# Optimization experiments

Hardware: AMD Instinct MI355X
Metric: run time of the kernel (lower is better)

Reference implementation:

```python
import jax, jax.numpy as jnp
import numpy as np

B, T, N, F = 32, 64, 128, 128
U, K1, K2 = 64, 64, 32
EPS = 1e-3  # keras BatchNormalization default epsilon
SLOPE = 0.01  # LeakyReLU negative_slope


def setup_inputs() -> dict:
    key = jax.random.key(0)
    ks = jax.random.split(key, 16)
    g = lambda k, sh, s=0.05: jax.random.normal(k, sh, dtype=jnp.float32) * s
    inp = {
        "x": jax.random.normal(ks[0], (B, T, F), dtype=jnp.float32),
        "a": jax.random.uniform(ks[1], (B, N, N), dtype=jnp.float32),
        # LSTM (keras gate order i, f, c, o)
        "lstm_k": g(ks[2], (F, 4 * U)),
        "lstm_r": g(ks[3], (U, 4 * U)),
        "lstm_b": jnp.zeros((4 * U,), jnp.float32),
        # BatchNorm params (inference form: gamma, beta, moving mean, moving var)
        "bnl_g": jnp.ones((U,), jnp.float32), "bnl_b": jnp.zeros((U,), jnp.float32),
        "bnl_m": jnp.zeros((U,), jnp.float32), "bnl_v": jnp.ones((U,), jnp.float32),
        "w1": g(ks[4], (U, K1)), "b1": jnp.zeros((K1,), jnp.float32),
        "bn1_g": jnp.ones((K1,), jnp.float32), "bn1_b": jnp.zeros((K1,), jnp.float32),
        "bn1_m": jnp.zeros((K1,), jnp.float32), "bn1_v": jnp.ones((K1,), jnp.float32),
        "w2": g(ks[5], (K1, K2)), "b2": jnp.zeros((K2,), jnp.float32),
        "bn2_g": jnp.ones((K2,), jnp.float32), "bn2_b": jnp.zeros((K2,), jnp.float32),
        "bn2_m": jnp.zeros((K2,), jnp.float32), "bn2_v": jnp.ones((K2,), jnp.float32),
        "d1_w": g(ks[6], (T * N * K2, 3), 0.01), "d1_b": jnp.zeros((3,), jnp.float32),
        "d2_w": g(ks[7], (3, N)), "d2_b": jnp.zeros((N,), jnp.float32),
    }
    return inp


def _bn(x, g, b, m, v):
    return (x - m) * (g * jax.lax.rsqrt(v + EPS)) + b


def _leaky(x):
    return jnp.where(x >= 0, x, SLOPE * x)


def _lstm(x, Wk, Wr, b):
    # x: [B, T, F] -> hs: [B, T, U]
    xz = jnp.einsum('btf,fg->btg', x, Wk) + b  # precompute input projections
    u = Wr.shape[0]
    h0 = jnp.zeros((x.shape[0], u), x.dtype)
    c0 = jnp.zeros((x.shape[0], u), x.dtype)

    def step(carry, zt):
        h, c = carry
        z = zt + h @ Wr
        i, f, g_, o = jnp.split(z, 4, axis=-1)
        i = jax.nn.sigmoid(i); f = jax.nn.sigmoid(f)
        g_ = jnp.tanh(g_); o = jax.nn.sigmoid(o)
        c = f * c + i * g_
        h = o * jnp.tanh(c)
        return (h, c), h

    _, hs = jax.lax.scan(step, (h0, c0), xz.transpose(1, 0, 2))
    return hs.transpose(1, 0, 2)


def reference(x, a, lstm_k, lstm_r, lstm_b, bnl_g, bnl_b, bnl_m, bnl_v,
              w1, b1, bn1_g, bn1_b, bn1_m, bn1_v,
              w2, b2, bn2_g, bn2_b, bn2_m, bn2_v,
              d1_w, d1_b, d2_w, d2_b):
    h = _lstm(x, lstm_k, lstm_r, lstm_b)              # [B, T, U]
    h = _bn(h, bnl_g, bnl_b, bnl_m, bnl_v)            # inference BN; dropout is identity
    # tile each timestep's LSTM output over the N nodes, then GCN1
    support1 = jnp.einsum('btu,uk->btk', h, w1)       # [B, T, K1] (identical across nodes)
    sup1 = jnp.broadcast_to(support1[:, :, None, :], (h.shape[0], h.shape[1], N, w1.shape[1]))
    g1 = jnp.einsum('bij,btjk->btik', a, sup1) + b1   # adjacency matmul
    g1 = _leaky(g1)
    g1 = _bn(g1, bn1_g, bn1_b, bn1_m, bn1_v)
    # GCN2
    sup2 = jnp.einsum('btnk,km->btnm', g1, w2)
    g2 = jnp.einsum('bij,btjm->btim', a, sup2) + b2
    g2 = _leaky(g2)
    g2 = _bn(g2, bn2_g, bn2_b, bn2_m, bn2_v)          # [B, T, N, K2]
    flat = g2.reshape(g2.shape[0], -1)                # [B, T*N*K2]
    d1 = jax.nn.relu(flat @ d1_w + d1_b)              # [B, 3]
    return d1 @ d2_w + d2_b                           # [B, N]
```

## Files before the change

kernel.cpp:

```cpp
#include <hip/hip_runtime.h>

#define BB 32
#define TT 64
#define NN 128
#define FF 128
#define UU 64
#define K1 64
#define K2 32
#define G4 256
#define EPSV 1e-3f
#define SLOPE 0.01f

#define ALD 136
#define SLD 136
#define WLD 72

typedef __attribute__((ext_vector_type(8))) short short8;
typedef __attribute__((ext_vector_type(4))) float f32x4;
typedef __attribute__((ext_vector_type(2))) __fp16 half2v;

__device__ __forceinline__ float sigmoidf_(float x) {
  return __builtin_amdgcn_rcpf(1.f + __expf(-x));
}
__device__ __forceinline__ float tanhf_(float x) {
  return 1.f - 2.f * __builtin_amdgcn_rcpf(__expf(2.f * x) + 1.f);
}
__device__ __forceinline__ float leaky_(float x) { return x >= 0.f ? x : SLOPE * x; }
__device__ __forceinline__ unsigned short f2bf(float x) {
  union { float f; unsigned u; } v; v.f = x;
  unsigned r = v.u + 0x7fff + ((v.u >> 16) & 1);
  return (unsigned short)(r >> 16);
}

__global__ __launch_bounds__(256) void k_pre(const float* __restrict__ x,
                                             const float* __restrict__ wk,
                                             const float* __restrict__ bias,
                                             const float* __restrict__ a,
                                             const float* __restrict__ w2,
                                             const float* __restrict__ wr,
                                             float* __restrict__ xz,
                                             float* __restrict__ rsum,
                                             unsigned short* __restrict__ apad,
                                             unsigned short* __restrict__ w2t,
                                             unsigned* __restrict__ wrp) {
  int tid = threadIdx.x;
  if (blockIdx.x < 32) {
    int b = blockIdx.x;
    int wave = tid >> 6, lane = tid & 63;
    const float* ab = a + (size_t)b * NN * NN;
    for (int r = 0; r < 32; ++r) {
      int row = wave * 32 + r;
      float2 v = *(const float2*)(ab + (size_t)row * NN + lane * 2);
      float s = v.x + v.y;
#pragma unroll
      for (int off = 32; off >= 1; off >>= 1) s += __shfl_down(s, off);
      if (lane == 0) rsum[b * NN + row] = s;
    }
    unsigned short* ap = apad + (size_t)b * NN * ALD;
    for (int idx = tid; idx < NN * NN; idx += 256) {
      int i = idx >> 7, j = idx & 127;
      ap[i * ALD + j] = f2bf(ab[idx]);
    }
    if (b == 0) {
      for (int idx = tid; idx < K1 * K2; idx += 256) {
        int k = idx >> 5, m = idx & 31;
        w2t[m * WLD + k] = f2bf(w2[idx]);
      }
    }
    if (b == 1) {
      for (int idx = tid; idx < 4 * 32 * UU; idx += 256) {
        int u2 = idx & 63;
        int p = (idx >> 6) & 31;
        int gate = idx >> 11;
        int col = gate * UU + u2;
        union { __fp16 h[2]; unsigned u; } pk;
        pk.h[0] = (__fp16)wr[(2 * p) * G4 + col];
        pk.h[1] = (__fp16)wr[(2 * p + 1) * G4 + col];
        wrp[idx] = pk.u;
      }
    }
  } else {
    __shared__ float xs[8][FF];
    int row0 = (blockIdx.x - 32) * 8;
    for (int i = tid; i < 8 * FF; i += 256) xs[i >> 7][i & 127] = x[(size_t)row0 * FF + i];
    __syncthreads();
    int g = tid;
    float acc[8];
    float bg = bias[g];
#pragma unroll
    for (int r = 0; r < 8; ++r) acc[r] = bg;
    for (int f = 0; f < FF; ++f) {
      float w = wk[f * G4 + g];
#pragma unroll
      for (int r = 0; r < 8; ++r) acc[r] += xs[r][f] * w;
    }
#pragma unroll
    for (int r = 0; r < 8; ++r) xz[(size_t)(row0 + r) * G4 + g] = acc[r];
  }
}

__global__ __launch_bounds__(64, 1) void k_lstm(const float* __restrict__ xz,
                                                const unsigned* __restrict__ wrp,
                                                const float* __restrict__ bnl_g,
                                                const float* __restrict__ bnl_b,
                                                const float* __restrict__ bnl_m,
                                                const float* __restrict__ bnl_v,
                                                float* __restrict__ hbn) {
  __shared__ __align__(16) float xz_lds[TT * G4];
  __shared__ __align__(16) __fp16 h16[UU];
  int u = threadIdx.x;
  int b = blockIdx.x;

  {
    const float4* src = (const float4*)(xz + (size_t)b * TT * G4);
    float4* dst = (float4*)xz_lds;
#pragma unroll
    for (int k = 0; k < 64; ++k) dst[u + k * 64] = src[u + k * 64];
  }
  unsigned wv[4][32];
#pragma unroll
  for (int gate = 0; gate < 4; ++gate)
#pragma unroll
    for (int p = 0; p < 32; ++p) wv[gate][p] = wrp[(gate * 32 + p) * UU + u];

  float bscale = bnl_g[u] * rsqrtf(bnl_v[u] + EPSV);
  float boff = bnl_b[u] - bnl_m[u] * bscale;
  h16[u] = (__fp16)0.f;
  float c = 0.f;
  float* hb = hbn + (size_t)b * TT * UU;

  for (int t = 0; t < TT; ++t) {
    unsigned hw[32];
    {
      const uint4* hq = (const uint4*)h16;
#pragma unroll
      for (int k = 0; k < 8; ++k) {
        uint4 v = hq[k];
        hw[4 * k + 0] = v.x; hw[4 * k + 1] = v.y; hw[4 * k + 2] = v.z; hw[4 * k + 3] = v.w;
      }
    }
    float zi = xz_lds[t * G4 + u];
    float zf = xz_lds[t * G4 + 64 + u];
    float zg = xz_lds[t * G4 + 128 + u];
    float zo = xz_lds[t * G4 + 192 + u];
#pragma unroll
    for (int p = 0; p < 32; ++p) {
      half2v hh = __builtin_bit_cast(half2v, hw[p]);
      zi = __builtin_amdgcn_fdot2(__builtin_bit_cast(half2v, wv[0][p]), hh, zi, false);
      zf = __builtin_amdgcn_fdot2(__builtin_bit_cast(half2v, wv[1][p]), hh, zf, false);
      zg = __builtin_amdgcn_fdot2(__builtin_bit_cast(half2v, wv[2][p]), hh, zg, false);
      zo = __builtin_amdgcn_fdot2(__builtin_bit_cast(half2v, wv[3][p]), hh, zo, false);
    }
    float i_ = sigmoidf_(zi), f_ = sigmoidf_(zf), g_ = tanhf_(zg), o_ = sigmoidf_(zo);
    c = f_ * c + i_ * g_;
    float h = o_ * tanhf_(c);
    h16[u] = (__fp16)h;
    hb[t * UU + u] = h * bscale + boff;
  }
}

__global__ __launch_bounds__(256) void k_gcn(
    const float* __restrict__ hbn, const float* __restrict__ w1,
    const float* __restrict__ rsum,
    const unsigned short* __restrict__ apad, const unsigned short* __restrict__ w2t,
    const float* __restrict__ b1,
    const float* __restrict__ bn1_g, const float* __restrict__ bn1_b,
    const float* __restrict__ bn1_m, const float* __restrict__ bn1_v,
    const float* __restrict__ b2,
    const float* __restrict__ bn2_g, const float* __restrict__ bn2_b,
    const float* __restrict__ bn2_m, const float* __restrict__ bn2_v,
    const float* __restrict__ d1w, float* __restrict__ part) {
  __shared__ unsigned short a_lds[NN * ALD];
  __shared__ unsigned short s2_lds[K2 * SLD];
  __shared__ unsigned short w2_lds[K2 * WLD];
  __shared__ float4 gp[K1];
  __shared__ float r_lds[NN];
  __shared__ float p2[3 * K2];
  __shared__ float red[12];

  int blk = blockIdx.x;
  int b = blk & 31, t = blk >> 5;
  int tid = threadIdx.x;
  int lane = tid & 63, wave = tid >> 6;
  int l15 = lane & 15, l4 = lane >> 4;

  {
    const uint4* src = (const uint4*)(apad + (size_t)b * NN * ALD);
    uint4* dst = (uint4*)a_lds;
    for (int i = tid; i < NN * ALD / 8; i += 256) dst[i] = src[i];
  }
  {
    const uint2* src = (const uint2*)w2t;
    uint2* dst = (uint2*)w2_lds;
    for (int i = tid; i < K2 * WLD / 4; i += 256) dst[i] = src[i];
  }
  if (tid < K1) {
    float hv = hbn[((size_t)b * TT + t) * UU + tid];
    float s1v = 0.f;
#pragma unroll
    for (int u = 0; u < UU; ++u) s1v += __shfl(hv, u) * w1[u * K1 + tid];
    float s = bn1_g[tid] * rsqrtf(bn1_v[tid] + EPSV);
    gp[tid] = make_float4(s1v, b1[tid], s, bn1_b[tid] - bn1_m[tid] * s);
  }
  if (tid >= 64 && tid < 64 + NN) r_lds[tid - 64] = rsum[b * NN + (tid - 64)];
  if (tid >= 192 && tid < 192 + K2) {
    int m = tid - 192;
    float s = bn2_g[m] * rsqrtf(bn2_v[m] + EPSV);
    p2[m] = b2[m];
    p2[K2 + m] = s;
    p2[2 * K2 + m] = bn2_b[m] - bn2_m[m] * s;
  }
  __syncthreads();

  f32x4 z4 = {0.f, 0.f, 0.f, 0.f};

  {
    float rj0 = r_lds[(wave * 2 + 0) * 16 + l15];
    float rj1 = r_lds[(wave * 2 + 1) * 16 + l15];
    f32x4 acc[2][2];
    acc[0][0] = z4; acc[0][1] = z4; acc[1][0] = z4; acc[1][1] = z4;
#pragma unroll
    for (int kt = 0; kt < 2; ++kt) {
      float4 gpv[8];
#pragma unroll
      for (int e = 0; e < 8; ++e) gpv[e] = gp[kt * 32 + l4 * 8 + e];
      short8 bfrag0 = *((const short8*)&w2_lds[(0 + l15) * WLD + kt * 32 + l4 * 8]);
      short8 bfrag1 = *((const short8*)&w2_lds[(16 + l15) * WLD + kt * 32 + l4 * 8]);
#pragma unroll
      for (int jt = 0; jt < 2; ++jt) {
        float rj = jt ? rj1 : rj0;
        short8 af;
#pragma unroll
        for (int e = 0; e < 8; ++e) {
          float4 p = gpv[e];
          float v = leaky_(rj * p.x + p.y) * p.z + p.w;
          af[e] = (short)f2bf(v);
        }
        acc[jt][0] = __builtin_amdgcn_mfma_f32_16x16x32_bf16(af, bfrag0, acc[jt][0], 0, 0, 0);
        acc[jt][1] = __builtin_amdgcn_mfma_f32_16x16x32_bf16(af, bfrag1, acc[jt][1], 0, 0, 0);
      }
    }
#pragma unroll
    for (int jt = 0; jt < 2; ++jt) {
      int jbase = (wave * 2 + jt) * 16 + l4 * 4;
#pragma unroll
      for (int mt = 0; mt < 2; ++mt) {
        int m = mt * 16 + l15;
        unsigned lo = (unsigned)f2bf(acc[jt][mt][0]) | ((unsigned)f2bf(acc[jt][mt][1]) << 16);
        unsigned hi = (unsigned)f2bf(acc[jt][mt][2]) | ((unsigned)f2bf(acc[jt][mt][3]) << 16);
        uint2 val; val.x = lo; val.y = hi;
        *((uint2*)&s2_lds[m * SLD + jbase]) = val;
      }
    }
  }
  __syncthreads();

  float c0 = 0.f, c1 = 0.f, c2 = 0.f;
  {
    f32x4 acc[2][2];
    acc[0][0] = z4; acc[0][1] = z4; acc[1][0] = z4; acc[1][1] = z4;
#pragma unroll
    for (int kt = 0; kt < 4; ++kt) {
      short8 bfrag0 = *((const short8*)&s2_lds[(0 + l15) * SLD + kt * 32 + l4 * 8]);
      short8 bfrag1 = *((const short8*)&s2_lds[(16 + l15) * SLD + kt * 32 + l4 * 8]);
#pragma unroll
      for (int it = 0; it < 2; ++it) {
        int i = (wave * 2 + it) * 16 + l15;
        short8 afrag = *((const short8*)&a_lds[i * ALD + kt * 32 + l4 * 8]);
        acc[it][0] = __builtin_amdgcn_mfma_f32_16x16x32_bf16(afrag, bfrag0, acc[it][0], 0, 0, 0);
        acc[it][1] = __builtin_amdgcn_mfma_f32_16x16x32_bf16(afrag, bfrag1, acc[it][1], 0, 0, 0);
      }
    }
    const float* dw = d1w + (size_t)t * NN * K2 * 3;
#pragma unroll
    for (int it = 0; it < 2; ++it) {
      int ibase = (wave * 2 + it) * 16 + l4 * 4;
#pragma unroll
      for (int mt = 0; mt < 2; ++mt) {
        int m = mt * 16 + l15;
        float bb = p2[m], bs = p2[K2 + m], bo = p2[2 * K2 + m];
#pragma unroll
        for (int r = 0; r < 4; ++r) {
          int i = ibase + r;
          float g2 = leaky_(acc[it][mt][r] + bb) * bs + bo;
          const float* dp = dw + ((size_t)i * K2 + m) * 3;
          c0 += g2 * dp[0];
          c1 += g2 * dp[1];
          c2 += g2 * dp[2];
        }
      }
    }
  }
#pragma unroll
  for (int off = 32; off >= 1; off >>= 1) {
    c0 += __shfl_down(c0, off);
    c1 += __shfl_down(c1, off);
    c2 += __shfl_down(c2, off);
  }
  if (lane == 0) { red[wave * 3 + 0] = c0; red[wave * 3 + 1] = c1; red[wave * 3 + 2] = c2; }
  __syncthreads();
  if (tid == 0) {
    float s0 = 0.f, s1v = 0.f, s2v = 0.f;
    for (int w = 0; w < 4; ++w) { s0 += red[w * 3]; s1v += red[w * 3 + 1]; s2v += red[w * 3 + 2]; }
    part[((size_t)b * TT + t) * 3 + 0] = s0;
    part[((size_t)b * TT + t) * 3 + 1] = s1v;
    part[((size_t)b * TT + t) * 3 + 2] = s2v;
  }
}

__global__ __launch_bounds__(128) void k_out(const float* __restrict__ part,
                                             const float* __restrict__ d1b,
                                             const float* __restrict__ d2w,
                                             const float* __restrict__ d2b,
                                             float* __restrict__ out) {
  int b = blockIdx.x, n = threadIdx.x;
  float s[3] = {0.f, 0.f, 0.f};
  const float* p = part + (size_t)b * TT * 3;
  for (int t = 0; t < TT; ++t) {
    s[0] += p[t * 3];
    s[1] += p[t * 3 + 1];
    s[2] += p[t * 3 + 2];
  }
  float o = d2b[n];
#pragma unroll
  for (int c = 0; c < 3; ++c) {
    float d = s[c] + d1b[c];
    d = d > 0.f ? d : 0.f;
    o += d * d2w[c * NN + n];
  }
  out[b * NN + n] = o;
}

extern "C" void kernel_launch(void* const* d_in, const int* in_sizes, int n_in,
                              void* d_out, int out_size, void* d_ws, size_t ws_size,
                              hipStream_t stream) {
  const float* x      = (const float*)d_in[0];
  const float* a      = (const float*)d_in[1];
  const float* lstm_k = (const float*)d_in[2];
  const float* lstm_r = (const float*)d_in[3];
  const float* lstm_b = (const float*)d_in[4];
  const float* bnl_g  = (const float*)d_in[5];
  const float* bnl_b  = (const float*)d_in[6];
  const float* bnl_m  = (const float*)d_in[7];
  const float* bnl_v  = (const float*)d_in[8];
  const float* w1     = (const float*)d_in[9];
  const float* b1     = (const float*)d_in[10];
  const float* bn1_g  = (const float*)d_in[11];
  const float* bn1_b  = (const float*)d_in[12];
  const float* bn1_m  = (const float*)d_in[13];
  const float* bn1_v  = (const float*)d_in[14];
  const float* w2     = (const float*)d_in[15];
  const float* b2     = (const float*)d_in[16];
  const float* bn2_g  = (const float*)d_in[17];
  const float* bn2_b  = (const float*)d_in[18];
  const float* bn2_m  = (const float*)d_in[19];
  const float* bn2_v  = (const float*)d_in[20];
  const float* d1_w   = (const float*)d_in[21];
  const float* d1_b   = (const float*)d_in[22];
  const float* d2_w   = (const float*)d_in[23];
  const float* d2_b   = (const float*)d_in[24];
  float* out = (float*)d_out;

  char* ws = (char*)d_ws;
  float* xz            = (float*)(ws + 0);
  float* hbn           = (float*)(ws + 2097152);
  float* rsum          = (float*)(ws + 2621440);
  float* part          = (float*)(ws + 2637824);
  unsigned short* apad = (unsigned short*)(ws + 2662400);
  unsigned short* w2t  = (unsigned short*)(ws + 3776512);
  unsigned* wrp        = (unsigned*)(ws + 3781120);

  k_pre<<<32 + BB * TT / 8, 256, 0, stream>>>(x, lstm_k, lstm_b, a, w2, lstm_r,
                                              xz, rsum, apad, w2t, wrp);
  k_lstm<<<BB, 64, 0, stream>>>(xz, wrp, bnl_g, bnl_b, bnl_m, bnl_v, hbn);
  k_gcn<<<BB * TT, 256, 0, stream>>>(hbn, w1, rsum, apad, w2t, b1, bn1_g, bn1_b, bn1_m, bn1_v,
                                     b2, bn2_g, bn2_b, bn2_m, bn2_v, d1_w, part);
  k_out<<<BB, 128, 0, stream>>>(part, d1_b, d2_w, d2_b, out);
}
```

Measured before the change: 80.31 us.

## Batch eight timesteps per GCN block and precompute support1 in separate kernel

The GCN kernel now handles eight timesteps per block (256 blocks instead of 2048), so the padded adjacency and W2 tiles are loaded into LDS once and reused eight times. The h@W1 projection moves out into a new k_s1 kernel, and the LSTM buffers its normalized outputs in LDS and writes them out with vectorized stores at the end. This cuts redundant global-to-LDS traffic for the adjacency matrix. In exchange it adds a launch, an extra global round trip for s1, and fewer blocks, which may leave many of the 256 compute units idle.

```diff
diff --git a/kernel.cpp b/kernel.cpp
--- a/kernel.cpp
+++ b/kernel.cpp
@@ -107,6 +107,7 @@
                                                 const float* __restrict__ bnl_v,
                                                 float* __restrict__ hbn) {
   __shared__ __align__(16) float xz_lds[TT * G4];
+  __shared__ __align__(16) float hist[TT * UU];
   __shared__ __align__(16) __fp16 h16[UU];
   int u = threadIdx.x;
   int b = blockIdx.x;
@@ -127,7 +128,6 @@
   float boff = bnl_b[u] - bnl_m[u] * bscale;
   h16[u] = (__fp16)0.f;
   float c = 0.f;
-  float* hb = hbn + (size_t)b * TT * UU;
 
   for (int t = 0; t < TT; ++t) {
     unsigned hw[32];
@@ -155,13 +155,34 @@
     c = f_ * c + i_ * g_;
     float h = o_ * tanhf_(c);
     h16[u] = (__fp16)h;
-    hb[t * UU + u] = h * bscale + boff;
-  }
+    hist[t * UU + u] = h * bscale + boff;
+  }
+  const float4* hs4 = (const float4*)hist;
+  float4* hb4 = (float4*)(hbn + (size_t)b * TT * UU);
+#pragma unroll
+  for (int k = 0; k < 16; ++k) hb4[u + k * 64] = hs4[u + k * 64];
+}
+
+__global__ __launch_bounds__(256) void k_s1(const float* __restrict__ hbn,
+                                            const float* __restrict__ w1,
+                                            float* __restrict__ s1) {
+  __shared__ float hs[16][UU];
+  int row0 = blockIdx.x * 16, tid = threadIdx.x;
+  for (int i = tid; i < 16 * UU; i += 256) hs[i >> 6][i & 63] = hbn[(size_t)row0 * UU + i];
+  __syncthreads();
+  int k = tid & 63, rg = tid >> 6;
+  float acc[4] = {0.f, 0.f, 0.f, 0.f};
+  for (int u = 0; u < UU; ++u) {
+    float w = w1[u * K1 + k];
+#pragma unroll
+    for (int rr = 0; rr < 4; ++rr) acc[rr] += hs[rg * 4 + rr][u] * w;
+  }
+#pragma unroll
+  for (int rr = 0; rr < 4; ++rr) s1[(size_t)(row0 + rg * 4 + rr) * K1 + k] = acc[rr];
 }
 
 __global__ __launch_bounds__(256) void k_gcn(
-    const float* __restrict__ hbn, const float* __restrict__ w1,
-    const float* __restrict__ rsum,
+    const float* __restrict__ s1g, const float* __restrict__ rsum,
     const unsigned short* __restrict__ apad, const unsigned short* __restrict__ w2t,
     const float* __restrict__ b1,
     const float* __restrict__ bn1_g, const float* __restrict__ bn1_b,
@@ -173,13 +194,14 @@
   __shared__ unsigned short a_lds[NN * ALD];
   __shared__ unsigned short s2_lds[K2 * SLD];
   __shared__ unsigned short w2_lds[K2 * WLD];
+  __shared__ float s1l[8][K1];
   __shared__ float4 gp[K1];
   __shared__ float r_lds[NN];
   __shared__ float p2[3 * K2];
   __shared__ float red[12];
 
   int blk = blockIdx.x;
-  int b = blk & 31, t = blk >> 5;
+  int tg = blk >> 5, b = blk & 31;
   int tid = threadIdx.x;
   int lane = tid & 63, wave = tid >> 6;
   int l15 = lane & 15, l4 = lane >> 4;
@@ -194,15 +216,14 @@
     uint2* dst = (uint2*)w2_lds;
     for (int i = tid; i < K2 * WLD / 4; i += 256) dst[i] = src[i];
   }
+  if (tid < 128) {
+    ((float4*)s1l)[tid] = ((const float4*)(s1g + ((size_t)b * TT + tg * 8) * K1))[tid];
+  }
   if (tid < K1) {
-    float hv = hbn[((size_t)b * TT + t) * UU + tid];
-    float s1v = 0.f;
-#pragma unroll
-    for (int u = 0; u < UU; ++u) s1v += __shfl(hv, u) * w1[u * K1 + tid];
     float s = bn1_g[tid] * rsqrtf(bn1_v[tid] + EPSV);
-    gp[tid] = make_float4(s1v, b1[tid], s, bn1_b[tid] - bn1_m[tid] * s);
-  }
-  if (tid >= 64 && tid < 64 + NN) r_lds[tid - 64] = rsum[b * NN + (tid - 64)];
+    gp[tid] = make_float4(b1[tid], s, bn1_b[tid] - bn1_m[tid] * s, 0.f);
+  }
+  if (tid < NN) r_lds[tid] = rsum[b * NN + tid];
   if (tid >= 192 && tid < 192 + K2) {
     int m = tid - 192;
     float s = bn2_g[m] * rsqrtf(bn2_v[m] + EPSV);
@@ -213,19 +234,30 @@
   __syncthreads();
 
   f32x4 z4 = {0.f, 0.f, 0.f, 0.f};
-
-  {
-    float rj0 = r_lds[(wave * 2 + 0) * 16 + l15];
-    float rj1 = r_lds[(wave * 2 + 1) * 16 + l15];
-    f32x4 acc[2][2];
-    acc[0][0] = z4; acc[0][1] = z4; acc[1][0] = z4; acc[1][1] = z4;
+  float rj0 = r_lds[(wave * 2 + 0) * 16 + l15];
+  float rj1 = r_lds[(wave * 2 + 1) * 16 + l15];
+  short8 bw[2][2];
+#pragma unroll
+  for (int kt = 0; kt < 2; ++kt) {
+    bw[kt][0] = *((const short8*)&w2_lds[(0 + l15) * WLD + kt * 32 + l4 * 8]);
+    bw[kt][1] = *((const short8*)&w2_lds[(16 + l15) * WLD + kt * 32 + l4 * 8]);
+  }
+
+  float c0 = 0.f, c1 = 0.f, c2 = 0.f;
+
+  for (int ti = 0; ti < 8; ++ti) {
+    int t = tg * 8 + ti;
+    f32x4 a1[2][2];
+    a1[0][0] = z4; a1[0][1] = z4; a1[1][0] = z4; a1[1][1] = z4;
 #pragma unroll
     for (int kt = 0; kt < 2; ++kt) {
       float4 gpv[8];
-#pragma unroll
-      for (int e = 0; e < 8; ++e) gpv[e] = gp[kt * 32 + l4 * 8 + e];
-      short8 bfrag0 = *((const short8*)&w2_lds[(0 + l15) * WLD + kt * 32 + l4 * 8]);
-      short8 bfrag1 = *((const short8*)&w2_lds[(16 + l15) * WLD + kt * 32 + l4 * 8]);
+      float s1v[8];
+#pragma unroll
+      for (int e = 0; e < 8; ++e) {
+        gpv[e] = gp[kt * 32 + l4 * 8 + e];
+        s1v[e] = s1l[ti][kt * 32 + l4 * 8 + e];
+      }
 #pragma unroll
       for (int jt = 0; jt < 2; ++jt) {
         float rj = jt ? rj1 : rj0;
@@ -233,30 +265,28 @@
 #pragma unroll
         for (int e = 0; e < 8; ++e) {
           float4 p = gpv[e];
-          float v = leaky_(rj * p.x + p.y) * p.z + p.w;
+          float v = leaky_(rj * s1v[e] + p.x) * p.y + p.z;
           af[e] = (short)f2bf(v);
         }
-        acc[jt][0] = __builtin_amdgcn_mfma_f32_16x16x32_bf16(af, bfrag0, acc[jt][0], 0, 0, 0);
-        acc[jt][1] = __builtin_amdgcn_mfma_f32_16x16x32_bf16(af, bfrag1, acc[jt][1], 0, 0, 0);
-      }
-    }
+        a1[jt][0] = __builtin_amdgcn_mfma_f32_16x16x32_bf16(af, bw[kt][0], a1[jt][0], 0, 0, 0);
+        a1[jt][1] = __builtin_amdgcn_mfma_f32_16x16x32_bf16(af, bw[kt][1], a1[jt][1], 0, 0, 0);
+      }
+    }
+    __syncthreads();
 #pragma unroll
     for (int jt = 0; jt < 2; ++jt) {
       int jbase = (wave * 2 + jt) * 16 + l4 * 4;
 #pragma unroll
       for (int mt = 0; mt < 2; ++mt) {
         int m = mt * 16 + l15;
-        unsigned lo = (unsigned)f2bf(acc[jt][mt][0]) | ((unsigned)f2bf(acc[jt][mt][1]) << 16);
-        unsigned hi = (unsigned)f2bf(acc[jt][mt][2]) | ((unsigned)f2bf(acc[jt][mt][3]) << 16);
+        unsigned lo = (unsigned)f2bf(a1[jt][mt][0]) | ((unsigned)f2bf(a1[jt][mt][1]) << 16);
+        unsigned hi = (unsigned)f2bf(a1[jt][mt][2]) | ((unsigned)f2bf(a1[jt][mt][3]) << 16);
         uint2 val; val.x = lo; val.y = hi;
         *((uint2*)&s2_lds[m * SLD + jbase]) = val;
       }
     }
-  }
-  __syncthreads();
-
-  float c0 = 0.f, c1 = 0.f, c2 = 0.f;
-  {
+    __syncthreads();
+
     f32x4 acc[2][2];
     acc[0][0] = z4; acc[0][1] = z4; acc[1][0] = z4; acc[1][1] = z4;
 #pragma unroll
@@ -291,6 +321,7 @@
       }
     }
   }
+
 #pragma unroll
   for (int off = 32; off >= 1; off >>= 1) {
     c0 += __shfl_down(c0, off);
@@ -302,9 +333,9 @@
   if (tid == 0) {
     float s0 = 0.f, s1v = 0.f, s2v = 0.f;
     for (int w = 0; w < 4; ++w) { s0 += red[w * 3]; s1v += red[w * 3 + 1]; s2v += red[w * 3 + 2]; }
-    part[((size_t)b * TT + t) * 3 + 0] = s0;
-    part[((size_t)b * TT + t) * 3 + 1] = s1v;
-    part[((size_t)b * TT + t) * 3 + 2] = s2v;
+    part[((size_t)b * 8 + tg) * 3 + 0] = s0;
+    part[((size_t)b * 8 + tg) * 3 + 1] = s1v;
+    part[((size_t)b * 8 + tg) * 3 + 2] = s2v;
   }
 }
 
@@ -315,11 +346,12 @@
                                              float* __restrict__ out) {
   int b = blockIdx.x, n = threadIdx.x;
   float s[3] = {0.f, 0.f, 0.f};
-  const float* p = part + (size_t)b * TT * 3;
-  for (int t = 0; t < TT; ++t) {
-    s[0] += p[t * 3];
-    s[1] += p[t * 3 + 1];
-    s[2] += p[t * 3 + 2];
+  const float* p = part + (size_t)b * 8 * 3;
+#pragma unroll
+  for (int g = 0; g < 8; ++g) {
+    s[0] += p[g * 3];
+    s[1] += p[g * 3 + 1];
+    s[2] += p[g * 3 + 2];
   }
   float o = d2b[n];
 #pragma unroll
@@ -364,16 +396,18 @@
   char* ws = (char*)d_ws;
   float* xz            = (float*)(ws + 0);
   float* hbn           = (float*)(ws + 2097152);
-  float* rsum          = (float*)(ws + 2621440);
-  float* part          = (float*)(ws + 2637824);
-  unsigned short* apad = (unsigned short*)(ws + 2662400);
-  unsigned short* w2t  = (unsigned short*)(ws + 3776512);
-  unsigned* wrp        = (unsigned*)(ws + 3781120);
+  float* s1            = (float*)(ws + 2621440);
+  float* rsum          = (float*)(ws + 3145728);
+  float* part          = (float*)(ws + 3162112);
+  unsigned short* apad = (unsigned short*)(ws + 3165184);
+  unsigned short* w2t  = (unsigned short*)(ws + 4279296);
+  unsigned* wrp        = (unsigned*)(ws + 4283904);
 
   k_pre<<<32 + BB * TT / 8, 256, 0, stream>>>(x, lstm_k, lstm_b, a, w2, lstm_r,
                                               xz, rsum, apad, w2t, wrp);
   k_lstm<<<BB, 64, 0, stream>>>(xz, wrp, bnl_g, bnl_b, bnl_m, bnl_v, hbn);
-  k_gcn<<<BB * TT, 256, 0, stream>>>(hbn, w1, rsum, apad, w2t, b1, bn1_g, bn1_b, bn1_m, bn1_v,
-                                     b2, bn2_g, bn2_b, bn2_m, bn2_v, d1_w, part);
+  k_s1<<<BB * TT / 16, 256, 0, stream>>>(hbn, w1, s1);
+  k_gcn<<<256, 256, 0, stream>>>(s1, rsum, apad, w2t, b1, bn1_g, bn1_b, bn1_m, bn1_v,
+                                 b2, bn2_g, bn2_b, bn2_m, bn2_v, d1_w, part);
   k_out<<<BB, 128, 0, stream>>>(part, d1_b, d2_w, d2_b, out);
 }
```

After: 91.05 us. +13.4%, slower.

## Move h@W1 projection into LSTM kernel and pre-permute d1 weights to fragment layout

Applied to the files above, without the earlier changes.

The LSTM kernel now runs with 256 threads: one wave does the recurrence and stores the BN-normalized h in LDS as fp16, then all four waves compute support1 = h@W1 with fdot2 and write it out. This removes the per-block shuffle-based 64x64 matvec from the GCN kernel. A new k_pre branch also rearranges d1_w into float4s matching the MFMA accumulator layout, so the GCN epilogue does coalesced vector loads instead of strided scalar loads of 3-wide rows. The cost is extra preprocessing blocks and an additional 3MB rearranged copy of d1_w on every call, and h is now fp16 before the W1 projection.

```diff
diff --git a/kernel.cpp b/kernel.cpp
--- a/kernel.cpp
+++ b/kernel.cpp
@@ -38,11 +38,15 @@
                                              const float* __restrict__ a,
                                              const float* __restrict__ w2,
                                              const float* __restrict__ wr,
+                                             const float* __restrict__ w1,
+                                             const float* __restrict__ d1w,
                                              float* __restrict__ xz,
                                              float* __restrict__ rsum,
                                              unsigned short* __restrict__ apad,
                                              unsigned short* __restrict__ w2t,
-                                             unsigned* __restrict__ wrp) {
+                                             unsigned* __restrict__ wrp,
+                                             unsigned* __restrict__ w1p,
+                                             float4* __restrict__ d1r) {
   int tid = threadIdx.x;
   if (blockIdx.x < 32) {
     int b = blockIdx.x;
@@ -79,7 +83,16 @@
         wrp[idx] = pk.u;
       }
     }
-  } else {
+    if (b == 2) {
+      for (int idx = tid; idx < 32 * K1; idx += 256) {
+        int k = idx & 63, p = idx >> 6;
+        union { __fp16 h[2]; unsigned u; } pk;
+        pk.h[0] = (__fp16)w1[(2 * p) * K1 + k];
+        pk.h[1] = (__fp16)w1[(2 * p + 1) * K1 + k];
+        w1p[idx] = pk.u;
+      }
+    }
+  } else if (blockIdx.x < 288) {
     __shared__ float xs[8][FF];
     int row0 = (blockIdx.x - 32) * 8;
     for (int i = tid; i < 8 * FF; i += 256) xs[i >> 7][i & 127] = x[(size_t)row0 * FF + i];
@@ -96,72 +109,125 @@
     }
 #pragma unroll
     for (int r = 0; r < 8; ++r) xz[(size_t)(row0 + r) * G4 + g] = acc[r];
-  }
-}
-
-__global__ __launch_bounds__(64, 1) void k_lstm(const float* __restrict__ xz,
-                                                const unsigned* __restrict__ wrp,
-                                                const float* __restrict__ bnl_g,
-                                                const float* __restrict__ bnl_b,
-                                                const float* __restrict__ bnl_m,
-                                                const float* __restrict__ bnl_v,
-                                                float* __restrict__ hbn) {
+  } else {
+    int blk2 = blockIdx.x - 288;
+#pragma unroll
+    for (int k = 0; k < 4; ++k) {
+      int F = (blk2 * 4 + k) * 256 + tid;
+      int L = F & 255;
+      int rem = F >> 8;
+      int c = rem % 3;
+      int rem2 = rem / 3;
+      int g = rem2 & 3;
+      int t = rem2 >> 2;
+      int it = g >> 1, mt = g & 1;
+      int wv = L >> 6, l = L & 63, l15v = l & 15, l4v = l >> 4;
+      int m = mt * 16 + l15v;
+      int ibase = (wv * 2 + it) * 16 + l4v * 4;
+      float4 v;
+      v.x = d1w[((size_t)t * 4096 + (ibase + 0) * 32 + m) * 3 + c];
+      v.y = d1w[((size_t)t * 4096 + (ibase + 1) * 32 + m) * 3 + c];
+      v.z = d1w[((size_t)t * 4096 + (ibase + 2) * 32 + m) * 3 + c];
+      v.w = d1w[((size_t)t * 4096 + (ibase + 3) * 32 + m) * 3 + c];
+      d1r[F] = v;
+    }
+  }
+}
+
+__global__ __launch_bounds__(256, 1) void k_lstm(const float* __restrict__ xz,
+                                                 const unsigned* __restrict__ wrp,
+                                                 const unsigned* __restrict__ w1p,
+                                                 const float* __restrict__ bnl_g,
+                                                 const float* __restrict__ bnl_b,
+                                                 const float* __restrict__ bnl_m,
+                                                 const float* __restrict__ bnl_v,
+                                                 float* __restrict__ s1out) {
   __shared__ __align__(16) float xz_lds[TT * G4];
+  __shared__ __align__(16) __fp16 hp[TT * UU];
   __shared__ __align__(16) __fp16 h16[UU];
-  int u = threadIdx.x;
+  int tid = threadIdx.x;
+  int wave = tid >> 6, lane = tid & 63;
   int b = blockIdx.x;
 
   {
     const float4* src = (const float4*)(xz + (size_t)b * TT * G4);
     float4* dst = (float4*)xz_lds;
 #pragma unroll
-    for (int k = 0; k < 64; ++k) dst[u + k * 64] = src[u + k * 64];
-  }
+    for (int k = 0; k < 16; ++k) dst[tid + k * 256] = src[tid + k * 256];
+  }
+  unsigned w1v[32];
+#pragma unroll
+  for (int p = 0; p < 32; ++p) w1v[p] = w1p[p * 64 + lane];
+
+  float bscale = bnl_g[lane] * rsqrtf(bnl_v[lane] + EPSV);
+  float boff = bnl_b[lane] - bnl_m[lane] * bscale;
+
   unsigned wv[4][32];
-#pragma unroll
-  for (int gate = 0; gate < 4; ++gate)
-#pragma unroll
-    for (int p = 0; p < 32; ++p) wv[gate][p] = wrp[(gate * 32 + p) * UU + u];
-
-  float bscale = bnl_g[u] * rsqrtf(bnl_v[u] + EPSV);
-  float boff = bnl_b[u] - bnl_m[u] * bscale;
-  h16[u] = (__fp16)0.f;
-  float c = 0.f;
-  float* hb = hbn + (size_t)b * TT * UU;
-
-  for (int t = 0; t < TT; ++t) {
-    unsigned hw[32];
+  if (wave == 0) {
+#pragma unroll
+    for (int gate = 0; gate < 4; ++gate)
+#pragma unroll
+      for (int p = 0; p < 32; ++p) wv[gate][p] = wrp[(gate * 32 + p) * UU + lane];
+    h16[lane] = (__fp16)0.f;
+  }
+  __syncthreads();
+
+  if (wave == 0) {
+    float c = 0.f;
+    for (int t = 0; t < TT; ++t) {
+      unsigned hw[32];
+      {
+        const uint4* hq = (const uint4*)h16;
+#pragma unroll
+        for (int k = 0; k < 8; ++k) {
+          uint4 v = hq[k];
+          hw[4 * k + 0] = v.x; hw[4 * k + 1] = v.y; hw[4 * k + 2] = v.z; hw[4 * k + 3] = v.w;
+        }
+      }
+      float zi = xz_lds[t * G4 + lane];
+      float zf = xz_lds[t * G4 + 64 + lane];
+      float zg = xz_lds[t * G4 + 128 + lane];
+      float zo = xz_lds[t * G4 + 192 + lane];
+#pragma unroll
+      for (int p = 0; p < 32; ++p) {
+        half2v hh = __builtin_bit_cast(half2v, hw[p]);
+        zi = __builtin_amdgcn_fdot2(__builtin_bit_cast(half2v, wv[0][p]), hh, zi, false);
+        zf = __builtin_amdgcn_fdot2(__builtin_bit_cast(half2v, wv[1][p]), hh, zf, false);
+        zg = __builtin_amdgcn_fdot2(__builtin_bit_cast(half2v, wv[2][p]), hh, zg, false);
+        zo = __builtin_amdgcn_fdot2(__builtin_bit_cast(half2v, wv[3][p]), hh, zo, false);
+      }
+      float i_ = sigmoidf_(zi), f_ = sigmoidf_(zf), g_ = tanhf_(zg), o_ = sigmoidf_(zo);
+      c = f_ * c + i_ * g_;
+      float h = o_ * tanhf_(c);
+      h16[lane] = (__fp16)h;
+      hp[t * UU + lane] = (__fp16)(h * bscale + boff);
+    }
+  }
+  __syncthreads();
+
+  float* s1b = s1out + (size_t)b * TT * K1;
+  for (int r = 0; r < 16; ++r) {
+    int t = wave * 16 + r;
+    unsigned hw2[32];
     {
-      const uint4* hq = (const uint4*)h16;
+      const uint4* hq = (const uint4*)(hp + t * UU);
 #pragma unroll
       for (int k = 0; k < 8; ++k) {
         uint4 v = hq[k];
-        hw[4 * k + 0] = v.x; hw[4 * k + 1] = v.y; hw[4 * k + 2] = v.z; hw[4 * k + 3] = v.w;
-      }
-    }
-    float zi = xz_lds[t * G4 + u];
-    float zf = xz_lds[t * G4 + 64 + u];
-    float zg = xz_lds[t * G4 + 128 + u];
-    float zo = xz_lds[t * G4 + 192 + u];
-#pragma unroll
-    for (int p = 0; p < 32; ++p) {
-      half2v hh = __builtin_bit_cast(half2v, hw[p]);
-      zi = __builtin_amdgcn_fdot2(__builtin_bit_cast(half2v, wv[0][p]), hh, zi, false);
-      zf = __builtin_amdgcn_fdot2(__builtin_bit_cast(half2v, wv[1][p]), hh, zf, false);
-      zg = __builtin_amdgcn_fdot2(__builtin_bit_cast(half2v, wv[2][p]), hh, zg, false);
-      zo = __builtin_amdgcn_fdot2(__builtin_bit_cast(half2v, wv[3][p]), hh, zo, false);
-    }
-    float i_ = sigmoidf_(zi), f_ = sigmoidf_(zf), g_ = tanhf_(zg), o_ = sigmoidf_(zo);
-    c = f_ * c + i_ * g_;
-    float h = o_ * tanhf_(c);
-    h16[u] = (__fp16)h;
-    hb[t * UU + u] = h * bscale + boff;
+        hw2[4 * k + 0] = v.x; hw2[4 * k + 1] = v.y; hw2[4 * k + 2] = v.z; hw2[4 * k + 3] = v.w;
+      }
+    }
+    float acc = 0.f;
+#pragma unroll
+    for (int p = 0; p < 32; ++p)
+      acc = __builtin_amdgcn_fdot2(__builtin_bit_cast(half2v, w1v[p]),
+                                   __builtin_bit_cast(half2v, hw2[p]), acc, false);
+    s1b[t * K1 + lane] = acc;
   }
 }
 
 __global__ __launch_bounds__(256) void k_gcn(
-    const float* __restrict__ hbn, const float* __restrict__ w1,
-    const float* __restrict__ rsum,
+    const float* __restrict__ s1g, const float* __restrict__ rsum,
     const unsigned short* __restrict__ apad, const unsigned short* __restrict__ w2t,
     const float* __restrict__ b1,
     const float* __restrict__ bn1_g, const float* __restrict__ bn1_b,
@@ -169,7 +235,7 @@
     const float* __restrict__ b2,
     const float* __restrict__ bn2_g, const float* __restrict__ bn2_b,
     const float* __restrict__ bn2_m, const float* __restrict__ bn2_v,
-    const float* __restrict__ d1w, float* __restrict__ part) {
+    const float4* __restrict__ d1r, float* __restrict__ part) {
   __shared__ unsigned short a_lds[NN * ALD];
   __shared__ unsigned short s2_lds[K2 * SLD];
   __shared__ unsigned short w2_lds[K2 * WLD];
@@ -195,10 +261,7 @@
     for (int i = tid; i < K2 * WLD / 4; i += 256) dst[i] = src[i];
   }
   if (tid < K1) {
-    float hv = hbn[((size_t)b * TT + t) * UU + tid];
-    float s1v = 0.f;
-#pragma unroll
-    for (int u = 0; u < UU; ++u) s1v += __shfl(hv, u) * w1[u * K1 + tid];
+    float s1v = s1g[((size_t)b * TT + t) * K1 + tid];
     float s = bn1_g[tid] * rsqrtf(bn1_v[tid] + EPSV);
     gp[tid] = make_float4(s1v, b1[tid], s, bn1_b[tid] - bn1_m[tid] * s);
   }
@@ -271,24 +334,25 @@
         acc[it][1] = __builtin_amdgcn_mfma_f32_16x16x32_bf16(afrag, bfrag1, acc[it][1], 0, 0, 0);
       }
     }
-    const float* dw = d1w + (size_t)t * NN * K2 * 3;
-#pragma unroll
-    for (int it = 0; it < 2; ++it) {
-      int ibase = (wave * 2 + it) * 16 + l4 * 4;
+    float gv[2][2][4];
+#pragma unroll
+    for (int it = 0; it < 2; ++it)
 #pragma unroll
       for (int mt = 0; mt < 2; ++mt) {
         int m = mt * 16 + l15;
         float bb = p2[m], bs = p2[K2 + m], bo = p2[2 * K2 + m];
 #pragma unroll
-        for (int r = 0; r < 4; ++r) {
-          int i = ibase + r;
-          float g2 = leaky_(acc[it][mt][r] + bb) * bs + bo;
-          const float* dp = dw + ((size_t)i * K2 + m) * 3;
-          c0 += g2 * dp[0];
-          c1 += g2 * dp[1];
-          c2 += g2 * dp[2];
-        }
-      }
+        for (int r = 0; r < 4; ++r) gv[it][mt][r] = leaky_(acc[it][mt][r] + bb) * bs + bo;
+      }
+#pragma unroll
+    for (int g = 0; g < 4; ++g) {
+      int it = g >> 1, mt = g & 1;
+      float4 v0 = d1r[(((size_t)t * 4 + g) * 3 + 0) * 256 + tid];
+      float4 v1 = d1r[(((size_t)t * 4 + g) * 3 + 1) * 256 + tid];
+      float4 v2 = d1r[(((size_t)t * 4 + g) * 3 + 2) * 256 + tid];
+      c0 += gv[it][mt][0] * v0.x + gv[it][mt][1] * v0.y + gv[it][mt][2] * v0.z + gv[it][mt][3] * v0.w;
+      c1 += gv[it][mt][0] * v1.x + gv[it][mt][1] * v1.y + gv[it][mt][2] * v1.z + gv[it][mt][3] * v1.w;
+      c2 += gv[it][mt][0] * v2.x + gv[it][mt][1] * v2.y + gv[it][mt][2] * v2.z + gv[it][mt][3] * v2.w;
     }
   }
 #pragma unroll
@@ -363,17 +427,19 @@
 
   char* ws = (char*)d_ws;
   float* xz            = (float*)(ws + 0);
-  float* hbn           = (float*)(ws + 2097152);
+  float* s1            = (float*)(ws + 2097152);
   float* rsum          = (float*)(ws + 2621440);
   float* part          = (float*)(ws + 2637824);
   unsigned short* apad = (unsigned short*)(ws + 2662400);
   unsigned short* w2t  = (unsigned short*)(ws + 3776512);
   unsigned* wrp        = (unsigned*)(ws + 3781120);
-
-  k_pre<<<32 + BB * TT / 8, 256, 0, stream>>>(x, lstm_k, lstm_b, a, w2, lstm_r,
-                                              xz, rsum, apad, w2t, wrp);
-  k_lstm<<<BB, 64, 0, stream>>>(xz, wrp, bnl_g, bnl_b, bnl_m, bnl_v, hbn);
-  k_gcn<<<BB * TT, 256, 0, stream>>>(hbn, w1, rsum, apad, w2t, b1, bn1_g, bn1_b, bn1_m, bn1_v,
-                                     b2, bn2_g, bn2_b, bn2_m, bn2_v, d1_w, part);
+  unsigned* w1p        = (unsigned*)(ws + 3813888);
+  float4* d1r          = (float4*)(ws + 3822080);
+
+  k_pre<<<480, 256, 0, stream>>>(x, lstm_k, lstm_b, a, w2, lstm_r, w1, d1_w,
+                                 xz, rsum, apad, w2t, wrp, w1p, d1r);
+  k_lstm<<<BB, 256, 0, stream>>>(xz, wrp, w1p, bnl_g, bnl_b, bnl_m, bnl_v, s1);
+  k_gcn<<<BB * TT, 256, 0, stream>>>(s1, rsum, apad, w2t, b1, bn1_g, bn1_b, bn1_m, bn1_v,
+                                     b2, bn2_g, bn2_b, bn2_m, bn2_v, d1r, part);
   k_out<<<BB, 128, 0, stream>>>(part, d1_b, d2_w, d2_b, out);
 }
```

Result: slower. 82.19 us (+2.3%).
